# Performance work log

Measured on AMD Instinct MI355X. Metric: run time of the kernel, lower is better.

## Reference

```python
import jax, jax.numpy as jnp
import numpy as np

W = 128    # window_size
NH = 8     # num_heads (hard-coded default in ArrowAttention/BiSPA)
NEG = -1e9


def _split_qkv(Wqkv, bqkv):
    Wq, Wk, Wv = jnp.split(Wqkv, 3, axis=1)
    bq, bk, bv = jnp.split(bqkv, 3)
    return (Wq, bq), (Wk, bk), (Wv, bv)


def cls_mha(x, Wqkv, bqkv, Wo, bo):
    # torch nn.MultiheadAttention with query = cls token, key = value = full sequence
    B, S, H = x.shape
    hd = H // NH
    (Wq, bq), (Wk, bk), (Wv, bv) = _split_qkv(Wqkv, bqkv)
    q = (x[:, :1] @ Wq + bq).reshape(B, 1, NH, hd)
    k = (x @ Wk + bk).reshape(B, S, NH, hd)
    v = (x @ Wv + bv).reshape(B, S, NH, hd)
    scores = jnp.einsum('bqhd,bkhd->bhqk', q, k) / jnp.sqrt(jnp.float32(hd))
    attn = jax.nn.softmax(scores, axis=-1)
    out = jnp.einsum('bhqk,bkhd->bqhd', attn, v).reshape(B, 1, H)
    return out @ Wo + bo


def windowed_mha(x, Wqkv, bqkv, Wo, bo, min_key):
    # Fused sliding-window MHA: token i attends to keys j with
    # max(min_key, i-W) <= j <= min(S-1, i+W). Implemented with a 3-block
    # banded layout instead of the original per-token Python loop of MHA calls.
    B, S, H = x.shape
    hd = H // NH
    (Wq, bq), (Wk, bk), (Wv, bv) = _split_qkv(Wqkv, bqkv)
    nb = (S + W - 1) // W
    Sp = nb * W
    pad = Sp - S

    def blk(t):  # [B,S,H] -> [B,nb,W,NH,hd]
        return jnp.pad(t, ((0, 0), (0, pad), (0, 0))).reshape(B, nb, W, NH, hd)

    qb = blk(x @ Wq + bq)
    kb = blk(x @ Wk + bk)
    vb = blk(x @ Wv + bv)

    def ctx(t):  # prev | cur | next block -> [B,nb,3W,NH,hd]
        tp = jnp.pad(t, ((0, 0), (1, 1), (0, 0), (0, 0), (0, 0)))
        return jnp.concatenate([tp[:, :-2], tp[:, 1:-1], tp[:, 2:]], axis=2)

    kc = ctx(kb)
    vc = ctx(vb)
    scores = jnp.einsum('bnqhd,bnkhd->bhnqk', qb, kc) / jnp.sqrt(jnp.float32(hd))
    # global positions of queries / context keys
    qpos = (jnp.arange(nb) * W)[:, None, None] + jnp.arange(W)[None, :, None]          # [nb,W,1]
    kpos = (jnp.arange(nb) * W - W)[:, None, None] + jnp.arange(3 * W)[None, None, :]  # [nb,1,3W]
    rel = kpos - qpos
    valid = (jnp.abs(rel) <= W) & (kpos >= min_key) & (kpos < S) & (qpos < S)
    scores = jnp.where(valid[None, None], scores, NEG)
    attn = jax.nn.softmax(scores, axis=-1)
    out = jnp.einsum('bhnqk,bnkhd->bnqhd', attn, vc).reshape(B, Sp, H)[:, :S]
    return out @ Wo + bo


def _sener_head(hidden_states,
                Wqkv_cls, bqkv_cls, Wo_cls, bo_cls,
                Wqkv_loc, bqkv_loc, Wo_loc, bo_loc,
                logn_scale,
                Wqkv_h, bqkv_h, Wo_h, bo_h,
                Wqkv_v, bqkv_v, Wo_v, bo_v,
                W1, b1, W2, b2, Wc, bc):
    # --- ArrowAttention ---
    global_out = cls_mha(hidden_states, Wqkv_cls, bqkv_cls, Wo_cls, bo_cls)          # [B,1,H]
    local_out = windowed_mha(hidden_states, Wqkv_loc, bqkv_loc, Wo_loc, bo_loc,
                             min_key=1)[:, 1:]                                       # [B,S-1,H]
    attended = jnp.concatenate([global_out, local_out], axis=1)                      # [B,S,H]
    # --- LogNScaling on cls token ---
    attended = jnp.concatenate([attended[:, :1] * logn_scale[0], attended[:, 1:]], axis=1)
    # --- BiSPA: two sliding-window attentions + MLP fusion ---
    h_out = windowed_mha(attended, Wqkv_h, bqkv_h, Wo_h, bo_h, min_key=0)
    v_out = windowed_mha(attended, Wqkv_v, bqkv_v, Wo_v, bo_v, min_key=0)
    combined = jnp.concatenate([h_out, v_out], axis=-1)                              # [B,S,2H]
    seq = jax.nn.relu(combined @ W1 + b1) @ W2 + b2                                  # [B,S,H]
    # dropout is identity in eval mode
    logits = seq @ Wc + bc                                                           # [B,S,L]
    return logits


def setup_inputs() -> dict:
    B, S, H, L = 2, 4096, 512, 17
    key = jax.random.key(0)
    ks = jax.random.split(key, 32)

    def p(k, shape):
        return (0.02 * jax.random.normal(k, shape)).astype(jnp.float32)

    inp = {
        'hidden_states': jax.random.normal(ks[0], (B, S, H), jnp.float32),
        'Wqkv_cls': p(ks[1], (H, 3 * H)), 'bqkv_cls': p(ks[2], (3 * H,)),
        'Wo_cls': p(ks[3], (H, H)), 'bo_cls': p(ks[4], (H,)),
        'Wqkv_loc': p(ks[5], (H, 3 * H)), 'bqkv_loc': p(ks[6], (3 * H,)),
        'Wo_loc': p(ks[7], (H, H)), 'bo_loc': p(ks[8], (H,)),
        'logn_scale': jnp.full((1,), 1.0 / np.sqrt(H), jnp.float32),
        'Wqkv_h': p(ks[9], (H, 3 * H)), 'bqkv_h': p(ks[10], (3 * H,)),
        'Wo_h': p(ks[11], (H, H)), 'bo_h': p(ks[12], (H,)),
        'Wqkv_v': p(ks[13], (H, 3 * H)), 'bqkv_v': p(ks[14], (3 * H,)),
        'Wo_v': p(ks[15], (H, H)), 'bo_v': p(ks[16], (H,)),
        'W1': p(ks[17], (2 * H, H)), 'b1': p(ks[18], (H,)),
        'W2': p(ks[19], (H, H)), 'b2': p(ks[20], (H,)),
        'Wc': p(ks[21], (H, L)), 'bc': p(ks[22], (L,)),
    }
    return inp


def reference(hidden_states,
              Wqkv_cls, bqkv_cls, Wo_cls, bo_cls,
              Wqkv_loc, bqkv_loc, Wo_loc, bo_loc,
              logn_scale,
              Wqkv_h, bqkv_h, Wo_h, bo_h,
              Wqkv_v, bqkv_v, Wo_v, bo_v,
              W1, b1, W2, b2, Wc, bc):
    return _sener_head(hidden_states,
                       Wqkv_cls, bqkv_cls, Wo_cls, bo_cls,
                       Wqkv_loc, bqkv_loc, Wo_loc, bo_loc,
                       logn_scale,
                       Wqkv_h, bqkv_h, Wo_h, bo_h,
                       Wqkv_v, bqkv_v, Wo_v, bo_v,
                       W1, b1, W2, b2, Wc, bc)
```

## Files before the change

kernel.cpp:

```cpp
#include <hip/hip_runtime.h>

#define S_ 4096
#define H_ 512
#define M_ 8192
#define CCH 8

typedef __attribute__((ext_vector_type(8))) short s16x8;
typedef __attribute__((ext_vector_type(4))) float f32x4;

__device__ __forceinline__ float bflo(unsigned int w) { return __uint_as_float(w << 16); }
__device__ __forceinline__ float bfhi(unsigned int w) { return __uint_as_float(w & 0xFFFF0000u); }
__device__ __forceinline__ float bf2f(unsigned short u) { return __uint_as_float(((unsigned int)u) << 16); }
__device__ __forceinline__ unsigned short f2bf(float f) {
    unsigned int x = __float_as_uint(f);
    return (unsigned short)((x + 0x7FFFu + ((x >> 16) & 1u)) >> 16);
}
__device__ __forceinline__ void gload_lds16(const void* g, void* l) {
    __builtin_amdgcn_global_load_lds(
        (const __attribute__((address_space(1))) unsigned int*)g,
        (__attribute__((address_space(3))) unsigned int*)l, 16, 0, 0);
}

__global__ __launch_bounds__(256) void cvt_kernel(
    const float* __restrict__ in, unsigned short* __restrict__ out, int n8)
{
    int i = blockIdx.x * 256 + threadIdx.x;
    if (i >= n8) return;
    float4 a = *(const float4*)(in + (size_t)i * 8);
    float4 b = *(const float4*)(in + (size_t)i * 8 + 4);
    uint4 pk;
    pk.x = (unsigned int)f2bf(a.x) | ((unsigned int)f2bf(a.y) << 16);
    pk.y = (unsigned int)f2bf(a.z) | ((unsigned int)f2bf(a.w) << 16);
    pk.z = (unsigned int)f2bf(b.x) | ((unsigned int)f2bf(b.y) << 16);
    pk.w = (unsigned int)f2bf(b.z) | ((unsigned int)f2bf(b.w) << 16);
    *(uint4*)(out + (size_t)i * 8) = pk;
}

__global__ __launch_bounds__(256) void wtrans_kernel(
    const float* __restrict__ p0, const float* __restrict__ p1,
    const float* __restrict__ p2, const float* __restrict__ p3,
    const float* __restrict__ p4,
    unsigned short* o0, unsigned short* o1,
    unsigned short* o2, unsigned short* o3, unsigned short* o4,
    int K, int N)
{
    const float* in; unsigned short* out;
    switch (blockIdx.z) {
        case 0:  in = p0; out = o0; break;
        case 1:  in = p1; out = o1; break;
        case 2:  in = p2; out = o2; break;
        case 3:  in = p3; out = o3; break;
        default: in = p4; out = o4; break;
    }
    __shared__ float tile[32][33];
    int n0 = blockIdx.x * 32, k0 = blockIdx.y * 32;
    int tx = threadIdx.x & 31, ty = threadIdx.x >> 5;
    #pragma unroll
    for (int i = 0; i < 4; ++i) {
        int k = k0 + ty * 4 + i;
        tile[ty * 4 + i][tx] = in[(size_t)k * N + n0 + tx];
    }
    __syncthreads();
    #pragma unroll
    for (int i = 0; i < 4; ++i) {
        int n = n0 + ty * 4 + i;
        out[(size_t)n * K + k0 + tx] = f2bf(tile[tx][ty * 4 + i]);
    }
}

template<int BM, int RELU>
__global__ __launch_bounds__(256) void mgemm_kernel(
    const unsigned short* __restrict__ A, int lda,
    const unsigned short* __restrict__ Bt, int ldb,
    const float* __restrict__ bias, const float* __restrict__ biasB, int nsplit,
    unsigned short* __restrict__ C, int ldc, int K,
    size_t az, size_t bz, size_t cz)
{
    constexpr int MF = BM / 32;
    constexpr int ASEG = BM / 32;
    __shared__ __align__(16) unsigned short As[BM * 64];
    __shared__ __align__(16) unsigned short Bs[128 * 64];
    const int z = blockIdx.z;
    A  += (size_t)z * az;
    Bt += (size_t)z * bz;
    C  += (size_t)z * cz;
    if (z > 0) bias = biasB;
    const int t = threadIdx.x;
    const int w = t >> 6, l = t & 63;
    const int wr = w >> 1, wc = w & 1;
    const int row0 = blockIdx.y * BM, col0 = blockIdx.x * 128;
    const int lr = l >> 3;
    const int lc = l & 7;

    f32x4 acc[MF][4];
    #pragma unroll
    for (int i = 0; i < MF; ++i)
        #pragma unroll
        for (int j = 0; j < 4; ++j) acc[i][j] = {0.f, 0.f, 0.f, 0.f};

    for (int k0 = 0; k0 < K; k0 += 64) {
        __syncthreads();
        #pragma unroll
        for (int i = 0; i < ASEG; ++i) {
            int seg = w * ASEG + i;
            int r = seg * 8 + lr;
            int kc = lc ^ (r & 7);
            gload_lds16(A + (size_t)(row0 + r) * lda + k0 + kc * 8,
                        (void*)(As + seg * 512));
        }
        #pragma unroll
        for (int i = 0; i < 4; ++i) {
            int seg = w * 4 + i;
            int r = seg * 8 + lr;
            int kc = lc ^ (r & 7);
            gload_lds16(Bt + (size_t)(col0 + r) * ldb + k0 + kc * 8,
                        (void*)(Bs + seg * 512));
        }
        __syncthreads();

        s16x8 af[MF][2], bf[4][2];
        #pragma unroll
        for (int mf = 0; mf < MF; ++mf)
            #pragma unroll
            for (int kk = 0; kk < 2; ++kk) {
                int r = wr * (BM / 2) + mf * 16 + (l & 15);
                int ch = (kk * 4 + (l >> 4)) ^ (r & 7);
                af[mf][kk] = *(const s16x8*)(As + r * 64 + ch * 8);
            }
        #pragma unroll
        for (int nf = 0; nf < 4; ++nf)
            #pragma unroll
            for (int kk = 0; kk < 2; ++kk) {
                int r = wc * 64 + nf * 16 + (l & 15);
                int ch = (kk * 4 + (l >> 4)) ^ (r & 7);
                bf[nf][kk] = *(const s16x8*)(Bs + r * 64 + ch * 8);
            }
        #pragma unroll
        for (int kk = 0; kk < 2; ++kk)
            #pragma unroll
            for (int mf = 0; mf < MF; ++mf)
                #pragma unroll
                for (int nf = 0; nf < 4; ++nf)
                    acc[mf][nf] = __builtin_amdgcn_mfma_f32_16x16x32_bf16(
                        af[mf][kk], bf[nf][kk], acc[mf][nf], 0, 0, 0);
    }

    #pragma unroll
    for (int mf = 0; mf < MF; ++mf)
        #pragma unroll
        for (int nf = 0; nf < 4; ++nf) {
            int col = col0 + wc * 64 + nf * 16 + (l & 15);
            float bb = (col < nsplit) ? bias[col] : biasB[col - nsplit];
            #pragma unroll
            for (int r4 = 0; r4 < 4; ++r4) {
                int row = row0 + wr * (BM / 2) + mf * 16 + (l >> 4) * 4 + r4;
                float v = acc[mf][nf][r4] + bb;
                if (RELU) v = fmaxf(v, 0.f);
                C[(size_t)row * ldc + col] = f2bf(v);
            }
        }
}

__global__ __launch_bounds__(256) void wattn_kernel(
    const unsigned short* __restrict__ qkv, int qld, int qbase,
    unsigned short* __restrict__ out, size_t brstride, int min_key)
{
    const int n = blockIdx.x, h = blockIdx.y;
    const int z = blockIdx.z, br = z >> 1, b = z & 1;
    const int t = threadIdx.x;
    const int w = t >> 6, l = t & 63;
    const int l4 = l >> 4, lm = l & 15;

    __shared__ __align__(16) unsigned short Ks[64 * 64];
    __shared__ __align__(16) unsigned short Vt[64 * 72];
    __shared__ __align__(16) unsigned short Ps[64 * 72];

    const int q0g = n * 64;
    const int qcol = qbase + br * 1536;
    const size_t base = (size_t)b * S_ * qld;
    out += (size_t)br * brstride;

    s16x8 qf[2];
    {
        const unsigned short* qrow =
            qkv + base + (size_t)(q0g + w * 16 + lm) * qld + qcol + h * 64 + l4 * 8;
        qf[0] = *(const s16x8*)(qrow);
        qf[1] = *(const s16x8*)(qrow + 32);
    }

    float m[4], lsum[4];
    f32x4 oacc[4];
    #pragma unroll
    for (int e = 0; e < 4; ++e) {
        m[e] = -1e30f; lsum[e] = 0.f;
        oacc[e] = {0.f, 0.f, 0.f, 0.f};
    }

    const int lr = l >> 3, lc = l & 7;

    for (int c = 0; c < 5; ++c) {
        const int klo = q0g - 128 + c * 64;
        if (klo < 0 || klo >= S_) continue;
        const bool need_mask = (c == 0) | (c == 4) | (klo < min_key);
        __syncthreads();

        #pragma unroll
        for (int i = 0; i < 2; ++i) {
            int seg = w * 2 + i;
            int r = seg * 8 + lr;
            int kc = lc ^ (r & 7);
            gload_lds16(qkv + base + (size_t)(klo + r) * qld + qcol + 512 + h * 64 + kc * 8,
                        (void*)(Ks + seg * 512));
        }
        {
            int jp = (t & 31) * 2, ds = (t >> 5) * 8;
            uint4 r0 = *(const uint4*)(qkv + base + (size_t)(klo + jp) * qld + qcol + 1024 + h * 64 + ds);
            uint4 r1 = *(const uint4*)(qkv + base + (size_t)(klo + jp + 1) * qld + qcol + 1024 + h * 64 + ds);
            const unsigned short* va = (const unsigned short*)&r0;
            const unsigned short* vb = (const unsigned short*)&r1;
            #pragma unroll
            for (int j = 0; j < 8; ++j)
                *(unsigned int*)(Vt + (ds + j) * 72 + jp) =
                    (unsigned int)va[j] | ((unsigned int)vb[j] << 16);
        }
        __syncthreads();

        f32x4 sf[4];
        #pragma unroll
        for (int nf = 0; nf < 4; ++nf) sf[nf] = {0.f, 0.f, 0.f, 0.f};
        #pragma unroll
        for (int kk = 0; kk < 2; ++kk)
            #pragma unroll
            for (int nf = 0; nf < 4; ++nf) {
                int r = nf * 16 + lm;
                int ch = (kk * 4 + l4) ^ (r & 7);
                s16x8 kf = *(const s16x8*)(Ks + r * 64 + ch * 8);
                sf[nf] = __builtin_amdgcn_mfma_f32_16x16x32_bf16(qf[kk], kf, sf[nf], 0, 0, 0);
            }

        #pragma unroll
        for (int r4 = 0; r4 < 4; ++r4) {
            const int qpos = q0g + w * 16 + l4 * 4 + r4;
            float sv[4];
            #pragma unroll
            for (int nf = 0; nf < 4; ++nf) sv[nf] = sf[nf][r4] * 0.125f;
            if (need_mask) {
                #pragma unroll
                for (int nf = 0; nf < 4; ++nf) {
                    int kpos = klo + nf * 16 + lm;
                    int rel = kpos - qpos;
                    bool valid = (rel <= 128) & (rel >= -128) & (kpos >= min_key);
                    if (!valid) sv[nf] = -1e9f;
                }
            }
            float mx = fmaxf(fmaxf(sv[0], sv[1]), fmaxf(sv[2], sv[3]));
            #pragma unroll
            for (int st = 1; st < 16; st <<= 1)
                mx = fmaxf(mx, __shfl_xor(mx, st, 64));
            float mn = fmaxf(m[r4], mx);
            float sc = __expf(m[r4] - mn);
            float ps = 0.f;
            #pragma unroll
            for (int nf = 0; nf < 4; ++nf) {
                sv[nf] = __expf(sv[nf] - mn);
                ps += sv[nf];
            }
            #pragma unroll
            for (int st = 1; st < 16; st <<= 1)
                ps += __shfl_xor(ps, st, 64);
            lsum[r4] = lsum[r4] * sc + ps;
            m[r4] = mn;
            #pragma unroll
            for (int nf = 0; nf < 4; ++nf) oacc[nf][r4] *= sc;
            const int prow = w * 16 + l4 * 4 + r4;
            #pragma unroll
            for (int nf = 0; nf < 4; ++nf)
                Ps[prow * 72 + nf * 16 + lm] = f2bf(sv[nf]);
        }

        #pragma unroll
        for (int kk = 0; kk < 2; ++kk) {
            s16x8 pf = *(const s16x8*)(Ps + (w * 16 + lm) * 72 + l4 * 8 + kk * 32);
            #pragma unroll
            for (int nf = 0; nf < 4; ++nf) {
                s16x8 vf = *(const s16x8*)(Vt + (nf * 16 + lm) * 72 + l4 * 8 + kk * 32);
                oacc[nf] = __builtin_amdgcn_mfma_f32_16x16x32_bf16(pf, vf, oacc[nf], 0, 0, 0);
            }
        }
    }

    #pragma unroll
    for (int r4 = 0; r4 < 4; ++r4) {
        float inv = 1.f / lsum[r4];
        size_t row = (size_t)b * S_ + q0g + w * 16 + l4 * 4 + r4;
        #pragma unroll
        for (int nf = 0; nf < 4; ++nf)
            out[row * 512 + h * 64 + nf * 16 + lm] = f2bf(oacc[nf][r4] * inv);
    }
}

__global__ __launch_bounds__(256) void qcls_kernel(
    const unsigned short* __restrict__ xb, const unsigned short* __restrict__ WqkvT,
    const float* __restrict__ bqkv, float* __restrict__ q_cls)
{
    int gw = blockIdx.x * 4 + (threadIdx.x >> 6);
    int l = threadIdx.x & 63;
    int b = gw >> 9, j = gw & 511;
    s16x8 xv = *(const s16x8*)(xb + (size_t)b * S_ * H_ + l * 8);
    s16x8 wv = *(const s16x8*)(WqkvT + (size_t)j * 512 + l * 8);
    float s = 0.f;
    #pragma unroll
    for (int e = 0; e < 8; ++e)
        s += bf2f((unsigned short)xv[e]) * bf2f((unsigned short)wv[e]);
    #pragma unroll
    for (int st = 1; st < 64; st <<= 1) s += __shfl_xor(s, st, 64);
    if (l == 0) q_cls[gw] = s + bqkv[j];
}

__global__ __launch_bounds__(256) void cls_attn_part(
    const float* __restrict__ q_cls, const unsigned short* __restrict__ qkv,
    float* __restrict__ part)
{
    const int bh = blockIdx.x, ck = blockIdx.y;
    const int b = bh >> 3, h = bh & 7;
    const int t = threadIdx.x;
    __shared__ float sQ[64];
    __shared__ float sP[512];
    __shared__ float red[256];
    __shared__ float pacc[16][64];
    if (t < 64) sQ[t] = q_cls[b * H_ + h * 64 + t] * 0.125f;
    __syncthreads();
    const size_t base = (size_t)b * S_ * 2560;
    const int j0 = ck * 512;

    float sv[2], smax = -1e30f;
    #pragma unroll
    for (int i = 0; i < 2; ++i) {
        int j = j0 + t + i * 256;
        const unsigned short* kr = qkv + base + (size_t)j * 2560 + h * 64;
        float s = 0.f;
        #pragma unroll
        for (int d8 = 0; d8 < 8; ++d8) {
            uint4 raw = *(const uint4*)(kr + d8 * 8);
            const float* q = &sQ[d8 * 8];
            s = fmaf(q[0], bflo(raw.x), s); s = fmaf(q[1], bfhi(raw.x), s);
            s = fmaf(q[2], bflo(raw.y), s); s = fmaf(q[3], bfhi(raw.y), s);
            s = fmaf(q[4], bflo(raw.z), s); s = fmaf(q[5], bfhi(raw.z), s);
            s = fmaf(q[6], bflo(raw.w), s); s = fmaf(q[7], bfhi(raw.w), s);
        }
        sv[i] = s;
        smax = fmaxf(smax, s);
    }
    red[t] = smax; __syncthreads();
    for (int st = 128; st > 0; st >>= 1) {
        if (t < st) red[t] = fmaxf(red[t], red[t + st]);
        __syncthreads();
    }
    float mc = red[0];
    __syncthreads();
    float ls = 0.f;
    #pragma unroll
    for (int i = 0; i < 2; ++i) {
        float p = __expf(sv[i] - mc);
        sP[t + i * 256] = p;
        ls += p;
    }
    red[t] = ls; __syncthreads();
    for (int st = 128; st > 0; st >>= 1) {
        if (t < st) red[t] += red[t + st];
        __syncthreads();
    }
    float lc = red[0];

    int g = t >> 4, d4 = t & 15;
    float4 acc; acc.x = 0.f; acc.y = 0.f; acc.z = 0.f; acc.w = 0.f;
    for (int j = g * 32; j < g * 32 + 32; ++j) {
        float p = sP[j];
        uint2 raw = *(const uint2*)(qkv + base + (size_t)(j0 + j) * 2560 + 512 + h * 64 + d4 * 4);
        acc.x = fmaf(p, bflo(raw.x), acc.x); acc.y = fmaf(p, bfhi(raw.x), acc.y);
        acc.z = fmaf(p, bflo(raw.y), acc.z); acc.w = fmaf(p, bfhi(raw.y), acc.w);
    }
    *(float4*)&pacc[g][d4 * 4] = acc;
    __syncthreads();
    float* op = part + (size_t)(bh * CCH + ck) * 66;
    if (t < 64) {
        float r = 0.f;
        #pragma unroll
        for (int g2 = 0; g2 < 16; ++g2) r += pacc[g2][t];
        op[t] = r;
    }
    if (t == 64) op[64] = mc;
    if (t == 65) op[65] = lc;
}

__global__ __launch_bounds__(64) void cls_attn_reduce(
    const float* __restrict__ part, float* __restrict__ gpre)
{
    int bh = blockIdx.x, t = threadIdx.x;
    int b = bh >> 3, h = bh & 7;
    const float* pp = part + (size_t)bh * CCH * 66;
    float M = -1e30f;
    #pragma unroll
    for (int c = 0; c < CCH; ++c) M = fmaxf(M, pp[c * 66 + 64]);
    float L = 0.f, o = 0.f;
    #pragma unroll
    for (int c = 0; c < CCH; ++c) {
        float wgt = __expf(pp[c * 66 + 64] - M);
        L += pp[c * 66 + 65] * wgt;
        o += pp[c * 66 + t] * wgt;
    }
    gpre[b * H_ + h * 64 + t] = o / L;
}

__global__ __launch_bounds__(256) void clsproj_kernel(
    const float* __restrict__ gpre, const unsigned short* __restrict__ WoT,
    const float* __restrict__ bo, const float* __restrict__ logn,
    unsigned short* __restrict__ attended)
{
    int gw = blockIdx.x * 4 + (threadIdx.x >> 6);
    int l = threadIdx.x & 63;
    int b = gw >> 9, j = gw & 511;
    const float* gr = gpre + b * H_ + l * 8;
    s16x8 wv = *(const s16x8*)(WoT + (size_t)j * 512 + l * 8);
    float s = 0.f;
    #pragma unroll
    for (int e = 0; e < 8; ++e) s += gr[e] * bf2f((unsigned short)wv[e]);
    #pragma unroll
    for (int st = 1; st < 64; st <<= 1) s += __shfl_xor(s, st, 64);
    if (l == 0) attended[(size_t)b * S_ * H_ + j] = f2bf((s + bo[j]) * logn[0]);
}

__global__ __launch_bounds__(256) void logits_kernel(
    const unsigned short* __restrict__ seq, const float* __restrict__ Wc,
    const float* __restrict__ bc, float* __restrict__ out)
{
    __shared__ float sWc[17][516];
    for (int i = threadIdx.x; i < 512 * 17; i += 256) {
        int d = i / 17, lcol = i % 17;
        sWc[lcol][d] = Wc[i];
    }
    __syncthreads();
    int idx = blockIdx.x * 256 + threadIdx.x;
    if (idx >= M_ * 17) return;
    int r = idx / 17, lcol = idx % 17;
    const unsigned short* sr = seq + (size_t)r * H_;
    float s = bc[lcol];
    for (int d8 = 0; d8 < 64; ++d8) {
        uint4 raw = *(const uint4*)(sr + d8 * 8);
        const float* wr = &sWc[lcol][d8 * 8];
        s = fmaf(bflo(raw.x), wr[0], s); s = fmaf(bfhi(raw.x), wr[1], s);
        s = fmaf(bflo(raw.y), wr[2], s); s = fmaf(bfhi(raw.y), wr[3], s);
        s = fmaf(bflo(raw.z), wr[4], s); s = fmaf(bfhi(raw.z), wr[5], s);
        s = fmaf(bflo(raw.w), wr[6], s); s = fmaf(bfhi(raw.w), wr[7], s);
    }
    out[idx] = s;
}

extern "C" void kernel_launch(void* const* d_in, const int* in_sizes, int n_in,
                              void* d_out, int out_size, void* d_ws, size_t ws_size,
                              hipStream_t stream) {
    const float* x        = (const float*)d_in[0];
    const float* Wqkv_cls = (const float*)d_in[1];
    const float* bqkv_cls = (const float*)d_in[2];
    const float* Wo_cls   = (const float*)d_in[3];
    const float* bo_cls   = (const float*)d_in[4];
    const float* Wqkv_loc = (const float*)d_in[5];
    const float* bqkv_loc = (const float*)d_in[6];
    const float* Wo_loc   = (const float*)d_in[7];
    const float* bo_loc   = (const float*)d_in[8];
    const float* logn     = (const float*)d_in[9];
    const float* Wqkv_h   = (const float*)d_in[10];
    const float* bqkv_h   = (const float*)d_in[11];
    const float* Wo_h     = (const float*)d_in[12];
    const float* bo_h     = (const float*)d_in[13];
    const float* Wqkv_v   = (const float*)d_in[14];
    const float* bqkv_v   = (const float*)d_in[15];
    const float* Wo_v     = (const float*)d_in[16];
    const float* bo_v     = (const float*)d_in[17];
    const float* W1       = (const float*)d_in[18];
    const float* b1       = (const float*)d_in[19];
    const float* W2       = (const float*)d_in[20];
    const float* b2       = (const float*)d_in[21];
    const float* Wc       = (const float*)d_in[22];
    const float* bc       = (const float*)d_in[23];
    float* out = (float*)d_out;

    unsigned short* wsu = (unsigned short*)d_ws;
    unsigned short* xb        = wsu;
    unsigned short* qkvA      = wsu +  4194304;
    unsigned short* qkvB      = wsu + 25165824;
    unsigned short* attnout_h = wsu + 50331648;
    unsigned short* attnout_v = wsu + 54525952;
    unsigned short* attended  = wsu + 58720256;
    unsigned short* combined  = wsu + 62914560;
    unsigned short* hidden    = wsu + 71303168;
    unsigned short* seq       = attended;
    unsigned short* WqkvT_cls = wsu + 75497472;
    unsigned short* WqkvT_loc = wsu + 76283904;
    unsigned short* WqkvT_h   = wsu + 77070336;
    unsigned short* WqkvT_v   = wsu + 77856768;
    unsigned short* WoT_loc   = wsu + 78643200;
    unsigned short* WoT_h     = wsu + 78905344;
    unsigned short* WoT_v     = wsu + 79167488;
    unsigned short* W2T       = wsu + 79429632;
    unsigned short* W1T       = wsu + 79691776;
    unsigned short* WoT_cls   = wsu + 80216064;
    float* q_cls              = (float*)(wsu + 80478208);
    float* gpre               = q_cls + 1024;
    float* part               = gpre + 1024;

    const int NSP_NONE = 1 << 30;
    dim3 blk(256);

    cvt_kernel<<<dim3(2048), blk, 0, stream>>>(x, xb, 524288);
    wtrans_kernel<<<dim3(48, 16, 4), blk, 0, stream>>>(
        Wqkv_cls, Wqkv_loc, Wqkv_h, Wqkv_v, Wqkv_cls,
        WqkvT_cls, WqkvT_loc, WqkvT_h, WqkvT_v, WqkvT_cls, 512, 1536);
    wtrans_kernel<<<dim3(16, 16, 5), blk, 0, stream>>>(
        Wo_loc, Wo_h, Wo_v, W2, Wo_cls,
        WoT_loc, WoT_h, WoT_v, W2T, WoT_cls, 512, 512);
    wtrans_kernel<<<dim3(16, 32, 1), blk, 0, stream>>>(
        W1, W1, W1, W1, W1,
        W1T, W1T, W1T, W1T, W1T, 1024, 512);

    mgemm_kernel<128, 0><<<dim3(20, 64), blk, 0, stream>>>(
        xb, 512, WqkvT_cls + 512 * 512, 512,
        bqkv_cls + 512, bqkv_loc, 1024, qkvA, 2560, 512, 0, 0, 0);

    qcls_kernel<<<dim3(256), blk, 0, stream>>>(xb, WqkvT_cls, bqkv_cls, q_cls);
    cls_attn_part<<<dim3(16, CCH), blk, 0, stream>>>(q_cls, qkvA, part);
    cls_attn_reduce<<<dim3(16), dim3(64), 0, stream>>>(part, gpre);

    wattn_kernel<<<dim3(64, 8, 2), blk, 0, stream>>>(
        qkvA, 2560, 1024, attnout_h, 0, 1);
    mgemm_kernel<64, 0><<<dim3(4, 128), blk, 0, stream>>>(
        attnout_h, 512, WoT_loc, 512, bo_loc, bo_loc, NSP_NONE,
        attended, 512, 512, 0, 0, 0);
    clsproj_kernel<<<dim3(256), blk, 0, stream>>>(gpre, WoT_cls, bo_cls, logn, attended);

    mgemm_kernel<128, 0><<<dim3(24, 64), blk, 0, stream>>>(
        attended, 512, WqkvT_h, 512,
        bqkv_h, bqkv_v, 1536, qkvB, 3072, 512, 0, 0, 0);

    wattn_kernel<<<dim3(64, 8, 4), blk, 0, stream>>>(
        qkvB, 3072, 0, attnout_h, 4194304, 0);

    mgemm_kernel<64, 0><<<dim3(4, 128, 2), blk, 0, stream>>>(
        attnout_h, 512, WoT_h, 512, bo_h, bo_v, NSP_NONE,
        combined, 1024, 512, 4194304, 262144, 512);

    mgemm_kernel<64, 1><<<dim3(4, 128), blk, 0, stream>>>(
        combined, 1024, W1T, 1024, b1, b1, NSP_NONE, hidden, 512, 1024, 0, 0, 0);
    mgemm_kernel<64, 0><<<dim3(4, 128), blk, 0, stream>>>(
        hidden, 512, W2T, 512, b2, b2, NSP_NONE, seq, 512, 512, 0, 0, 0);
    logits_kernel<<<dim3((M_ * 17 + 255) / 256), blk, 0, stream>>>(seq, Wc, bc, out);
}
```

Baseline: 336.4 us.

## Transpose score MFMA in windowed attention and use lazy softmax rescaling

The windowed attention kernel now computes S^T by swapping the MFMA operands, so each lane owns a single query row. Row max and sum reductions drop to two cross-lane shuffles instead of four-step butterflies per row. The 1/sqrt(d) scale is folded into Q at load time, and rescaling of the running max is skipped when the new max stays within a threshold of the old one. P is written to LDS as packed 64-bit stores, and block indices are permuted to change the order blocks are scheduled in. Folding the scale into Q adds one extra bf16 rounding, and the lazy max allows exponentials up to e^8 before rescaling.

```diff
diff --git a/kernel.cpp b/kernel.cpp
--- a/kernel.cpp
+++ b/kernel.cpp
@@ -165,7 +165,9 @@
     const unsigned short* __restrict__ qkv, int qld, int qbase,
     unsigned short* __restrict__ out, size_t brstride, int min_key)
 {
-    const int n = blockIdx.x, h = blockIdx.y;
+    const int nb = blockIdx.x;
+    const int n = ((nb & 7) << 3) | (nb >> 3);
+    const int h = blockIdx.y;
     const int z = blockIdx.z, br = z >> 1, b = z & 1;
     const int t = threadIdx.x;
     const int w = t >> 6, l = t & 63;
@@ -186,15 +188,17 @@
             qkv + base + (size_t)(q0g + w * 16 + lm) * qld + qcol + h * 64 + l4 * 8;
         qf[0] = *(const s16x8*)(qrow);
         qf[1] = *(const s16x8*)(qrow + 32);
-    }
-
-    float m[4], lsum[4];
+        #pragma unroll
+        for (int e = 0; e < 8; ++e) {
+            qf[0][e] = (short)f2bf(bf2f((unsigned short)qf[0][e]) * 0.125f);
+            qf[1][e] = (short)f2bf(bf2f((unsigned short)qf[1][e]) * 0.125f);
+        }
+    }
+
+    float m_r = -1e30f, lsum = 0.f;
     f32x4 oacc[4];
     #pragma unroll
-    for (int e = 0; e < 4; ++e) {
-        m[e] = -1e30f; lsum[e] = 0.f;
-        oacc[e] = {0.f, 0.f, 0.f, 0.f};
-    }
+    for (int e = 0; e < 4; ++e) oacc[e] = {0.f, 0.f, 0.f, 0.f};
 
     const int lr = l >> 3, lc = l & 7;
 
@@ -235,48 +239,63 @@
                 int r = nf * 16 + lm;
                 int ch = (kk * 4 + l4) ^ (r & 7);
                 s16x8 kf = *(const s16x8*)(Ks + r * 64 + ch * 8);
-                sf[nf] = __builtin_amdgcn_mfma_f32_16x16x32_bf16(qf[kk], kf, sf[nf], 0, 0, 0);
+                sf[nf] = __builtin_amdgcn_mfma_f32_16x16x32_bf16(kf, qf[kk], sf[nf], 0, 0, 0);
             }
 
-        #pragma unroll
-        for (int r4 = 0; r4 < 4; ++r4) {
-            const int qpos = q0g + w * 16 + l4 * 4 + r4;
-            float sv[4];
-            #pragma unroll
-            for (int nf = 0; nf < 4; ++nf) sv[nf] = sf[nf][r4] * 0.125f;
-            if (need_mask) {
-                #pragma unroll
-                for (int nf = 0; nf < 4; ++nf) {
-                    int kpos = klo + nf * 16 + lm;
+        float sv[4][4];
+        #pragma unroll
+        for (int nf = 0; nf < 4; ++nf)
+            #pragma unroll
+            for (int r = 0; r < 4; ++r) {
+                float xv = sf[nf][r];
+                if (need_mask) {
+                    int kpos = klo + nf * 16 + l4 * 4 + r;
+                    int qpos = q0g + w * 16 + lm;
                     int rel = kpos - qpos;
                     bool valid = (rel <= 128) & (rel >= -128) & (kpos >= min_key);
-                    if (!valid) sv[nf] = -1e9f;
+                    if (!valid) xv = -1e9f;
                 }
+                sv[nf][r] = xv;
             }
-            float mx = fmaxf(fmaxf(sv[0], sv[1]), fmaxf(sv[2], sv[3]));
-            #pragma unroll
-            for (int st = 1; st < 16; st <<= 1)
-                mx = fmaxf(mx, __shfl_xor(mx, st, 64));
-            float mn = fmaxf(m[r4], mx);
-            float sc = __expf(m[r4] - mn);
-            float ps = 0.f;
-            #pragma unroll
-            for (int nf = 0; nf < 4; ++nf) {
-                sv[nf] = __expf(sv[nf] - mn);
-                ps += sv[nf];
-            }
-            #pragma unroll
-            for (int st = 1; st < 16; st <<= 1)
-                ps += __shfl_xor(ps, st, 64);
-            lsum[r4] = lsum[r4] * sc + ps;
-            m[r4] = mn;
-            #pragma unroll
-            for (int nf = 0; nf < 4; ++nf) oacc[nf][r4] *= sc;
-            const int prow = w * 16 + l4 * 4 + r4;
+        float mx01 = fmaxf(fmaxf(sv[0][0], sv[0][1]), fmaxf(sv[0][2], sv[0][3]));
+        float mx11 = fmaxf(fmaxf(sv[1][0], sv[1][1]), fmaxf(sv[1][2], sv[1][3]));
+        float mx21 = fmaxf(fmaxf(sv[2][0], sv[2][1]), fmaxf(sv[2][2], sv[2][3]));
+        float mx31 = fmaxf(fmaxf(sv[3][0], sv[3][1]), fmaxf(sv[3][2], sv[3][3]));
+        float mx = fmaxf(fmaxf(mx01, mx11), fmaxf(mx21, mx31));
+        mx = fmaxf(mx, __shfl_xor(mx, 16, 64));
+        mx = fmaxf(mx, __shfl_xor(mx, 32, 64));
+
+        if (!__all(mx <= m_r + 8.f)) {
+            float mn = fmaxf(m_r, mx);
+            float sc = __expf(m_r - mn);
+            lsum *= sc;
+            m_r = mn;
+            float sco[4];
+            #pragma unroll
+            for (int r4 = 0; r4 < 4; ++r4)
+                sco[r4] = __shfl(sc, l4 * 4 + r4, 64);
             #pragma unroll
             for (int nf = 0; nf < 4; ++nf)
-                Ps[prow * 72 + nf * 16 + lm] = f2bf(sv[nf]);
-        }
+                #pragma unroll
+                for (int r4 = 0; r4 < 4; ++r4) oacc[nf][r4] *= sco[r4];
+        }
+
+        float ps = 0.f;
+        #pragma unroll
+        for (int nf = 0; nf < 4; ++nf) {
+            float p0 = __expf(sv[nf][0] - m_r);
+            float p1 = __expf(sv[nf][1] - m_r);
+            float p2 = __expf(sv[nf][2] - m_r);
+            float p3 = __expf(sv[nf][3] - m_r);
+            ps += (p0 + p1) + (p2 + p3);
+            uint2 pk;
+            pk.x = (unsigned int)f2bf(p0) | ((unsigned int)f2bf(p1) << 16);
+            pk.y = (unsigned int)f2bf(p2) | ((unsigned int)f2bf(p3) << 16);
+            *(uint2*)(Ps + (w * 16 + lm) * 72 + nf * 16 + l4 * 4) = pk;
+        }
+        ps += __shfl_xor(ps, 16, 64);
+        ps += __shfl_xor(ps, 32, 64);
+        lsum += ps;
 
         #pragma unroll
         for (int kk = 0; kk < 2; ++kk) {
@@ -289,13 +308,17 @@
         }
     }
 
+    float inv = 1.f / lsum;
+    float invo[4];
+    #pragma unroll
+    for (int r4 = 0; r4 < 4; ++r4)
+        invo[r4] = __shfl(inv, l4 * 4 + r4, 64);
     #pragma unroll
     for (int r4 = 0; r4 < 4; ++r4) {
-        float inv = 1.f / lsum[r4];
         size_t row = (size_t)b * S_ + q0g + w * 16 + l4 * 4 + r4;
         #pragma unroll
         for (int nf = 0; nf < 4; ++nf)
-            out[row * 512 + h * 64 + nf * 16 + lm] = f2bf(oacc[nf][r4] * inv);
+            out[row * 512 + h * 64 + nf * 16 + lm] = f2bf(oacc[nf][r4] * invo[r4]);
     }
 }
 
```

Result: faster. 329.8 us (-2.0%).
